# Performance work log

Hardware: AMD Instinct MI355X
Metric: run time of the kernel (lower is better)

The kernel has to match this reference:

```python
import jax, jax.numpy as jnp
import numpy as np

NUM_HEADS = 16

def setup_inputs() -> dict:
    key = jax.random.key(0)
    k1, k2, k3 = jax.random.split(key, 3)
    B, T, D = 4, 2048, 1024
    x = jax.random.normal(k1, (B, T, D), dtype=jnp.float32)
    # lecun_normal: std = 1/sqrt(fan_in)
    w = jax.random.normal(k2, (3 * D, D), dtype=jnp.float32) * (1.0 / np.sqrt(D))
    w_out = jax.random.normal(k3, (D, D), dtype=jnp.float32) * (1.0 / np.sqrt(D))
    return {"x": x, "w": w, "w_out": w_out}


def reference(x, w, w_out):
    B, T, D = x.shape
    H = NUM_HEADS
    L = D // H
    # qkv projection: (B,T,3D)
    q, k, v = jnp.split(jnp.matmul(x, w.T), 3, axis=2)
    # -> (T,B,H,L) time-major for the scan
    q = q.reshape(B, T, H, L).transpose(1, 0, 2, 3)
    k = k.reshape(B, T, H, L).transpose(1, 0, 2, 3)
    v = v.reshape(B, T, H, L).transpose(1, 0, 2, 3)
    scale = jax.lax.rsqrt(jnp.float32(L))
    k_exp = jnp.exp(k * scale) + 1e-6            # (T,B,H,L)
    k_norm = jnp.cumsum(k_exp, axis=0)           # causal normalizer
    qs = jax.nn.softmax(q * scale, axis=-1) / k_norm

    def step(carry, args):
        qs_t, k_t, v_t = args                    # each (B,H,L)
        # accumulate outer product k_t v_t^T into (B,H,L,L) state
        carry = carry + k_t[..., :, None] * v_t[..., None, :]
        y_t = jnp.einsum('bhl,bhlm->bhm', qs_t, carry)
        return carry, y_t

    init = jnp.zeros((B, H, L, L), dtype=x.dtype)
    _, y = jax.lax.scan(step, init, (qs, k_exp, v))   # y: (T,B,H,L)
    y = y.reshape(T, B, D).transpose(1, 0, 2)         # (B,T,D)
    return jnp.matmul(y, w_out)                       # Dense, no bias
```

## Files before the change

kernel.cpp:

```cpp
#include <hip/hip_runtime.h>
#include <math.h>

#define Bsz   4
#define Tsz   2048
#define Dsz   1024
#define Hsz   16
#define Lsz   64
#define BHsz  64
#define CH    64
#define NCH   32
#define QKVLD 3072
#define SCL   0.125f
#define QSC   512.0f
#define QSCI  (1.0f/512.0f)

typedef float  floatx4 __attribute__((ext_vector_type(4)));
typedef _Float16 half8 __attribute__((ext_vector_type(8)));
typedef _Float16 half4 __attribute__((ext_vector_type(4)));
typedef _Float16 half2v __attribute__((ext_vector_type(2)));

#define AS1 __attribute__((address_space(1)))
#define AS3 __attribute__((address_space(3)))

static __device__ __forceinline__ void gload_lds16(const void* g, void* l) {
  __builtin_amdgcn_global_load_lds((const AS1 unsigned int*)g,
                                   (AS3 unsigned int*)l, 16, 0, 0);
}

static __device__ __forceinline__ float wave_max64(float v) {
#pragma unroll
  for (int off = 1; off < 64; off <<= 1) v = fmaxf(v, __shfl_xor(v, off));
  return v;
}
static __device__ __forceinline__ float wave_sum64(float v) {
#pragma unroll
  for (int off = 1; off < 64; off <<= 1) v += __shfl_xor(v, off);
  return v;
}

__launch_bounds__(256)
__global__ void prep(const float* __restrict__ x, _Float16* __restrict__ xh,
                     const float* __restrict__ w, _Float16* __restrict__ wh,
                     const float* __restrict__ wo, _Float16* __restrict__ woT) {
  const int blk = blockIdx.x, tid = threadIdx.x;
  if (blk < 11264) {
    const float* in  = (blk < 8192) ? x : w;
    _Float16*   outp = (blk < 8192) ? xh : wh;
    const int bi = (blk < 8192) ? blk : blk - 8192;
    const int i = (bi * 256 + tid) * 4;
    float4 v = *(const float4*)(in + i);
    half4 h = { (_Float16)v.x, (_Float16)v.y, (_Float16)v.z, (_Float16)v.w };
    *(half4*)(outp + i) = h;
  } else {
    __shared__ float tile[32][33];
    const int bi = blk - 11264;
    const int bx = (bi & 31) * 32;
    const int by = (bi >> 5) * 32;
    const int tx = tid & 31, ty0 = tid >> 5;
#pragma unroll
    for (int p = 0; p < 4; p++) {
      const int ty = ty0 + p * 8;
      tile[ty][tx] = wo[(size_t)(by + ty) * 1024 + bx + tx];
    }
    __syncthreads();
#pragma unroll
    for (int p = 0; p < 4; p++) {
      const int ty = ty0 + p * 8;
      woT[(size_t)(bx + ty) * 1024 + by + tx] = (_Float16)tile[tx][ty];
    }
  }
}

__launch_bounds__(256)
__global__ void gemm_f16_bt_f32(const _Float16* __restrict__ A, const _Float16* __restrict__ B,
                                float* __restrict__ C, int M, int N, int K) {
  __shared__ _Float16 As[128][32];
  __shared__ _Float16 Bs[128][32];
  const int tid  = threadIdx.x;
  const int wave = tid >> 6, lane = tid & 63;
  const int flat = blockIdx.y * gridDim.x + blockIdx.x;
  const int xcd = flat & 7, g = flat >> 3;
  const int m0 = (xcd * 8 + (g & 7)) * 128;
  const int n0 = (g >> 3) * 128;
  const int wm = (wave >> 1) * 64, wn = (wave & 1) * 64;
  const int fr = lane & 15;
  const int fq = lane >> 4;
  const int lr = lane >> 2;
  const int lk = (lane & 3) * 8;

  floatx4 zero = {0.f, 0.f, 0.f, 0.f};
  floatx4 acc[4][4];
#pragma unroll
  for (int mt = 0; mt < 4; mt++)
#pragma unroll
    for (int nt = 0; nt < 4; nt++) acc[mt][nt] = zero;

  for (int k0 = 0; k0 < K; k0 += 32) {
    __syncthreads();
#pragma unroll
    for (int j = 0; j < 2; j++) {
      const int ia = wave * 2 + j;
      gload_lds16(A + (size_t)(m0 + ia * 16 + lr) * K + k0 + lk, &As[ia * 16][0]);
      gload_lds16(B + (size_t)(n0 + ia * 16 + lr) * K + k0 + lk, &Bs[ia * 16][0]);
    }
    __syncthreads();

    half8 af[4], bf[4];
#pragma unroll
    for (int i = 0; i < 4; i++) {
      af[i] = *(const half8*)&As[wm + i * 16 + fr][fq * 8];
      bf[i] = *(const half8*)&Bs[wn + i * 16 + fr][fq * 8];
    }
#pragma unroll
    for (int mt = 0; mt < 4; mt++)
#pragma unroll
      for (int nt = 0; nt < 4; nt++)
        acc[mt][nt] = __builtin_amdgcn_mfma_f32_16x16x32_f16(af[mt], bf[nt], acc[mt][nt], 0, 0, 0);
  }
#pragma unroll
  for (int mt = 0; mt < 4; mt++)
#pragma unroll
    for (int nt = 0; nt < 4; nt++)
#pragma unroll
      for (int r = 0; r < 4; r++) {
        const int row = m0 + wm + mt * 16 + fq * 4 + r;
        const int col = n0 + wn + nt * 16 + fr;
        C[(size_t)row * N + col] = acc[mt][nt][r];
      }
}

__launch_bounds__(256)
__global__ void gemm_f16_bt_c16(const _Float16* __restrict__ A, const _Float16* __restrict__ B,
                                _Float16* __restrict__ C, int M, int N, int K) {
  __shared__ _Float16 As[128][32];
  __shared__ _Float16 Bs[128][32];
  const int tid  = threadIdx.x;
  const int wave = tid >> 6, lane = tid & 63;
  const int flat = blockIdx.y * gridDim.x + blockIdx.x;
  const int xcd = flat & 7, g = flat >> 3;
  const int m0 = (xcd * 8 + (g & 7)) * 128;
  const int n0 = (g >> 3) * 128;
  const int wm = (wave >> 1) * 64, wn = (wave & 1) * 64;
  const int fr = lane & 15;
  const int fq = lane >> 4;
  const int lr = lane >> 2;
  const int lk = (lane & 3) * 8;
  const bool kreg = (n0 >= 1024) && (n0 < 2048);

  floatx4 zero = {0.f, 0.f, 0.f, 0.f};
  floatx4 acc[4][4];
#pragma unroll
  for (int mt = 0; mt < 4; mt++)
#pragma unroll
    for (int nt = 0; nt < 4; nt++) acc[mt][nt] = zero;

  for (int k0 = 0; k0 < K; k0 += 32) {
    __syncthreads();
#pragma unroll
    for (int j = 0; j < 2; j++) {
      const int ia = wave * 2 + j;
      gload_lds16(A + (size_t)(m0 + ia * 16 + lr) * K + k0 + lk, &As[ia * 16][0]);
      gload_lds16(B + (size_t)(n0 + ia * 16 + lr) * K + k0 + lk, &Bs[ia * 16][0]);
    }
    __syncthreads();

    half8 af[4], bf[4];
#pragma unroll
    for (int i = 0; i < 4; i++) {
      af[i] = *(const half8*)&As[wm + i * 16 + fr][fq * 8];
      bf[i] = *(const half8*)&Bs[wn + i * 16 + fr][fq * 8];
    }
#pragma unroll
    for (int mt = 0; mt < 4; mt++)
#pragma unroll
      for (int nt = 0; nt < 4; nt++)
        acc[mt][nt] = __builtin_amdgcn_mfma_f32_16x16x32_f16(af[mt], bf[nt], acc[mt][nt], 0, 0, 0);
  }
#pragma unroll
  for (int mt = 0; mt < 4; mt++)
#pragma unroll
    for (int nt = 0; nt < 4; nt++)
#pragma unroll
      for (int r = 0; r < 4; r++) {
        const int row = m0 + wm + mt * 16 + fq * 4 + r;
        const int col = n0 + wn + nt * 16 + fr;
        float v = acc[mt][nt][r];
        if (kreg) v = __expf(v * SCL) + 1e-6f;
        C[(size_t)row * N + col] = (_Float16)v;
      }
}

__launch_bounds__(256)
__global__ void chunk_kv(const _Float16* __restrict__ qkv, float* __restrict__ KV,
                         float* __restrict__ Ksum) {
  const int blk = blockIdx.x;
  const int bh = blk >> 3, cgrp = blk & 7;
  const int b = bh >> 4, h = bh & 15;
  const int tid = threadIdx.x;
  const int wave = tid >> 6, lane = tid & 63;
  const int fr = lane & 15, fq = lane >> 4;
  const int m2  = (tid & 31) * 2;
  const int tg8 = (tid >> 5) * 8;

  __shared__ __align__(16) _Float16 KxT[64][72];
  __shared__ __align__(16) _Float16 VT [64][72];

  for (int cc = 0; cc < 4; cc++) {
    const int c = cgrp * 4 + cc;
    const size_t base = ((size_t)(b * Tsz + c * CH)) * QKVLD + h * 64;
    __syncthreads();
    half8 klo, khi, vlo, vhi;
#pragma unroll
    for (int j = 0; j < 8; j++) {
      const int t = tg8 + j;
      half2v kk = *(const half2v*)(qkv + base + (size_t)t * QKVLD + 1024 + m2);
      klo[j] = kk[0]; khi[j] = kk[1];
      half2v vv = *(const half2v*)(qkv + base + (size_t)t * QKVLD + 2048 + m2);
      vlo[j] = vv[0]; vhi[j] = vv[1];
    }
    *(half8*)&KxT[m2][tg8]     = klo;
    *(half8*)&KxT[m2 + 1][tg8] = khi;
    *(half8*)&VT[m2][tg8]      = vlo;
    *(half8*)&VT[m2 + 1][tg8]  = vhi;
    __syncthreads();

    floatx4 acc[4];
#pragma unroll
    for (int j = 0; j < 4; j++) acc[j] = (floatx4){0.f, 0.f, 0.f, 0.f};
#pragma unroll
    for (int ks = 0; ks < 2; ks++) {
      half8 av = *(const half8*)&VT[wave * 16 + fr][ks * 32 + fq * 8];
#pragma unroll
      for (int j = 0; j < 4; j++) {
        half8 bv = *(const half8*)&KxT[j * 16 + fr][ks * 32 + fq * 8];
        acc[j] = __builtin_amdgcn_mfma_f32_16x16x32_f16(av, bv, acc[j], 0, 0, 0);
      }
    }
    float* KVp = KV + ((size_t)(bh * NCH + c)) * 4096;
#pragma unroll
    for (int j = 0; j < 4; j++)
#pragma unroll
      for (int r = 0; r < 4; r++)
        KVp[(wave * 16 + fq * 4 + r) * 64 + j * 16 + fr] = acc[j][r];

    if (tid < 64) {
      float s = 0.f;
      const half8* row = (const half8*)&KxT[tid][0];
#pragma unroll
      for (int j8 = 0; j8 < 8; j8++) {
        half8 v8 = row[j8];
#pragma unroll
        for (int j = 0; j < 8; j++) s += (float)v8[j];
      }
      Ksum[(bh * NCH + c) * 64 + tid] = s;
    }
  }
}

__launch_bounds__(256)
__global__ void prefix_kern(float* __restrict__ KV, float* __restrict__ Ksum) {
  const int tid = threadIdx.x;
  if (blockIdx.x < 256) {
    const int bh = blockIdx.x >> 2;
    const int e  = (blockIdx.x & 3) * 1024 + tid * 4;
    float4* p = (float4*)(KV + (size_t)bh * NCH * 4096 + e);
    float4 acc = {0.f, 0.f, 0.f, 0.f};
#pragma unroll 4
    for (int c = 0; c < NCH; c++) {
      float4 t = p[(size_t)c * 1024];
      p[(size_t)c * 1024] = acc;
      acc.x += t.x; acc.y += t.y; acc.z += t.z; acc.w += t.w;
    }
  } else {
    const int cid = (blockIdx.x - 256) * 256 + tid;
    const int bh = cid >> 4, l4 = cid & 15;
    float4* p = (float4*)(Ksum + (size_t)bh * NCH * 64) + l4;
    float4 acc = {0.f, 0.f, 0.f, 0.f};
#pragma unroll 4
    for (int c = 0; c < NCH; c++) {
      float4 t = p[c * 16];
      p[c * 16] = acc;
      acc.x += t.x; acc.y += t.y; acc.z += t.z; acc.w += t.w;
    }
  }
}

__launch_bounds__(256)
__global__ void chunk_y(const _Float16* __restrict__ qkv, const float* __restrict__ KV,
                        const float* __restrict__ Ksum, _Float16* __restrict__ Y) {
  const int bh = blockIdx.x, c = blockIdx.y;
  const int b = bh >> 4, h = bh & 15;
  const int tid = threadIdx.x;
  const int wave = tid >> 6, lane = tid & 63;
  const int fr = lane & 15, fq = lane >> 4;

  __shared__ __align__(16) _Float16 kxh[64][72];
  __shared__ __align__(16) _Float16 kxT[64][72];
  __shared__ __align__(16) _Float16 Ph[64][136];
  __shared__ __align__(16) _Float16 Bh[64][136];

  const size_t base = ((size_t)(b * Tsz + c * CH)) * QKVLD + h * 64;
  const float* KVp = KV + ((size_t)(bh * NCH + c)) * 4096;
  const int ksoff = (bh * NCH + c) * 64;

  _Float16 qreg[16];
#pragma unroll
  for (int i = 0; i < 16; i++)
    qreg[i] = qkv[base + (size_t)(wave * 16 + i) * QKVLD + lane];

  float ksb[4];
#pragma unroll
  for (int j = 0; j < 4; j++) ksb[j] = Ksum[ksoff + j * 16 + fr];

  {
    const int rr  = tid >> 3;
    const int sg8 = (tid & 7) * 8;
#pragma unroll
    for (int p = 0; p < 2; p++) {
      const int t = p * 32 + rr;
      *(half8*)&kxh[t][sg8] =
          *(const half8*)(qkv + base + (size_t)t * QKVLD + 1024 + sg8);
      *(half8*)&Ph[t][64 + sg8] =
          *(const half8*)(qkv + base + (size_t)t * QKVLD + 2048 + sg8);
    }
  }
  {
    const int m  = tid >> 2;
    const int l0 = (tid & 3) * 16;
#pragma unroll
    for (int q = 0; q < 2; q++) {
      float4 s0 = *(const float4*)(KVp + m * 64 + l0 + q * 8);
      float4 s1 = *(const float4*)(KVp + m * 64 + l0 + q * 8 + 4);
      half8 hh = { (_Float16)s0.x, (_Float16)s0.y, (_Float16)s0.z, (_Float16)s0.w,
                   (_Float16)s1.x, (_Float16)s1.y, (_Float16)s1.z, (_Float16)s1.w };
      *(half8*)&Bh[m][l0 + q * 8] = hh;
    }
  }
  __syncthreads();

  {
    const int l2  = (tid & 31) * 2;
    const int tg8 = (tid >> 5) * 8;
    half8 k0, k1, v0, v1;
#pragma unroll
    for (int j = 0; j < 8; j++) {
      const int t = tg8 + j;
      half2v kk = *(const half2v*)&kxh[t][l2];
      k0[j] = kk[0]; k1[j] = kk[1];
      half2v vv = *(const half2v*)&Ph[t][64 + l2];
      v0[j] = vv[0]; v1[j] = vv[1];
    }
    *(half8*)&kxT[l2][tg8]          = k0;
    *(half8*)&kxT[l2 + 1][tg8]      = k1;
    *(half8*)&Bh[l2][64 + tg8]      = v0;
    *(half8*)&Bh[l2 + 1][64 + tg8]  = v1;
  }
  __syncthreads();

  {
    floatx4 kacc[4];
#pragma unroll
    for (int j = 0; j < 4; j++) kacc[j] = (floatx4){0.f, 0.f, 0.f, 0.f};
#pragma unroll
    for (int ks = 0; ks < 2; ks++) {
      half8 af;
#pragma unroll
      for (int j = 0; j < 8; j++)
        af[j] = (ks * 32 + fq * 8 + j) <= (wave * 16 + fr) ? (_Float16)1.0f
                                                           : (_Float16)0.0f;
#pragma unroll
      for (int j = 0; j < 4; j++) {
        half8 bf = *(const half8*)&kxT[j * 16 + fr][ks * 32 + fq * 8];
        kacc[j] = __builtin_amdgcn_mfma_f32_16x16x32_f16(af, bf, kacc[j], 0, 0, 0);
      }
    }
    __syncthreads();
#pragma unroll
    for (int j = 0; j < 4; j++)
#pragma unroll
      for (int r = 0; r < 4; r++)
        kxT[wave * 16 + fq * 4 + r][j * 16 + fr] =
            (_Float16)(QSC / (ksb[j] + kacc[j][r]));
  }

#pragma unroll
  for (int i = 0; i < 16; i++) {
    const int t = wave * 16 + i;
    float v = (float)qreg[i] * SCL;
    float m = wave_max64(v);
    float e = __expf(v - m);
    float s = wave_sum64(e);
    Ph[t][lane] = (_Float16)((e / s) * (float)kxT[t][lane]);
  }
  __syncthreads();

  const int wm = (wave >> 1) * 32, wn = (wave & 1) * 32;
  {
    floatx4 a2[2][2];
#pragma unroll
    for (int mt = 0; mt < 2; mt++)
#pragma unroll
      for (int nt = 0; nt < 2; nt++) a2[mt][nt] = (floatx4){0.f, 0.f, 0.f, 0.f};
#pragma unroll
    for (int ks = 0; ks < 2; ks++) {
      half8 af[2], bf[2];
#pragma unroll
      for (int i = 0; i < 2; i++) {
        af[i] = *(const half8*)&Ph[wm + i * 16 + fr][ks * 32 + fq * 8];
        bf[i] = *(const half8*)&kxh[wn + i * 16 + fr][ks * 32 + fq * 8];
      }
#pragma unroll
      for (int mt = 0; mt < 2; mt++)
#pragma unroll
        for (int nt = 0; nt < 2; nt++)
          a2[mt][nt] = __builtin_amdgcn_mfma_f32_16x16x32_f16(af[mt], bf[nt], a2[mt][nt], 0, 0, 0);
    }
#pragma unroll
    for (int mt = 0; mt < 2; mt++)
#pragma unroll
      for (int nt = 0; nt < 2; nt++)
#pragma unroll
        for (int r = 0; r < 4; r++) {
          const int t = wm + mt * 16 + fq * 4 + r;
          const int s = wn + nt * 16 + fr;
          Ph[t][64 + s] = (_Float16)(s <= t ? a2[mt][nt][r] : 0.f);
        }
  }
  __syncthreads();

  {
    floatx4 acc[2][2];
#pragma unroll
    for (int mt = 0; mt < 2; mt++)
#pragma unroll
      for (int nt = 0; nt < 2; nt++) acc[mt][nt] = (floatx4){0.f, 0.f, 0.f, 0.f};
#pragma unroll
    for (int ks = 0; ks < 4; ks++) {
      half8 af[2], bf[2];
#pragma unroll
      for (int i = 0; i < 2; i++) {
        af[i] = *(const half8*)&Ph[wm + i * 16 + fr][ks * 32 + fq * 8];
        bf[i] = *(const half8*)&Bh[wn + i * 16 + fr][ks * 32 + fq * 8];
      }
#pragma unroll
      for (int mt = 0; mt < 2; mt++)
#pragma unroll
        for (int nt = 0; nt < 2; nt++)
          acc[mt][nt] = __builtin_amdgcn_mfma_f32_16x16x32_f16(af[mt], bf[nt], acc[mt][nt], 0, 0, 0);
    }
#pragma unroll
    for (int mt = 0; mt < 2; mt++)
#pragma unroll
      for (int nt = 0; nt < 2; nt++)
#pragma unroll
        for (int r = 0; r < 4; r++)
          kxh[wm + mt * 16 + fq * 4 + r][wn + nt * 16 + fr] =
              (_Float16)(acc[mt][nt][r] * QSCI);
  }
  __syncthreads();

  {
    const int ty = tid >> 2, sg = (tid & 3) * 16;
    _Float16* yrow = Y + (size_t)(b * Tsz + c * CH + ty) * Dsz + h * 64 + sg;
    *(half8*)(yrow)     = *(const half8*)&kxh[ty][sg];
    *(half8*)(yrow + 8) = *(const half8*)&kxh[ty][sg + 8];
  }
}

extern "C" void kernel_launch(void* const* d_in, const int* in_sizes, int n_in,
                              void* d_out, int out_size, void* d_ws, size_t ws_size,
                              hipStream_t stream) {
  const float* x     = (const float*)d_in[0];
  const float* w     = (const float*)d_in[1];
  const float* w_out = (const float*)d_in[2];
  float* out = (float*)d_out;

  _Float16* xh   = (_Float16*)d_ws;
  _Float16* Yh   = xh;
  _Float16* wh   = xh + (size_t)8192 * 1024;
  _Float16* woT  = wh + (size_t)3072 * 1024;
  _Float16* qkvh = woT + (size_t)1024 * 1024;
  float* KV   = (float*)(qkvh + (size_t)8192 * 3072);
  float* Ksum = KV + (size_t)BHsz * NCH * 4096;

  prep<<<12288, 256, 0, stream>>>(x, xh, w, wh, w_out, woT);

  gemm_f16_bt_c16<<<dim3(24, 64), 256, 0, stream>>>(xh, wh, qkvh, 8192, 3072, 1024);

  chunk_kv<<<512, 256, 0, stream>>>(qkvh, KV, Ksum);
  prefix_kern<<<260, 256, 0, stream>>>(KV, Ksum);
  chunk_y<<<dim3(BHsz, NCH), 256, 0, stream>>>(qkvh, KV, Ksum, Yh);

  gemm_f16_bt_f32<<<dim3(8, 64), 256, 0, stream>>>(Yh, woT, out, 8192, 1024, 1024);
}
```

Baseline: 257.7 us.

## Replace QKV projection GEMM with 256x256-tile double-buffered 8-wave pipelined kernel

Replaces the simple 128x128, K=32, single-buffered QKV GEMM with a 256x256-tile kernel that uses 512 threads, K=64 steps and two LDS buffers. Global-to-LDS loads for the next K slice are interleaved with the MFMA phases, and an XOR swizzle avoids LDS bank conflicts. The intent is to raise arithmetic intensity and hide memory latency in the largest GEMM. The cost is high register pressure from 32 accumulators per thread, large LDS use (128KB per block), and a hard-coded shape with a fragile hand-written wait/barrier schedule.

```diff
diff --git a/kernel.cpp b/kernel.cpp
--- a/kernel.cpp
+++ b/kernel.cpp
@@ -71,6 +71,127 @@
   }
 }
 
+__launch_bounds__(512, 2)
+__global__ void qkv_gemm8(const _Float16* __restrict__ A, const _Float16* __restrict__ B,
+                          _Float16* __restrict__ C) {
+  __shared__ __align__(16) _Float16 AsF[2 * 256 * 64];
+  __shared__ __align__(16) _Float16 BsF[2 * 256 * 64];
+  const int tid  = threadIdx.x;
+  const int wv   = tid >> 6, lane = tid & 63;
+  const int wm   = wv >> 2, wn = wv & 3;
+  const int fr   = lane & 15, fq = lane >> 4;
+
+  const int flat = blockIdx.x;
+  const int g  = (flat & 7) * 48 + (flat >> 3);
+  const int m0 = (g / 12) * 256;
+  const int n0 = (g % 12) * 256;
+
+  const int srow = lane >> 3;
+  const int scg  = (lane & 7) ^ srow;
+  const int wv8  = wv * 8;
+  const _Float16* aSrc = A + (size_t)(m0 + wv8 + srow) * 1024 + scg * 8;
+  const _Float16* bSrc = B + (size_t)(n0 + wv8 + srow) * 1024 + scg * 8;
+
+  const int sw  = fr & 7;
+  const int ck0 = ((0 + fq) ^ sw) * 8;
+  const int ck1 = ((4 + fq) ^ sw) * 8;
+  const _Float16* apt = AsF + (wm * 64 + fr) * 64;
+  const _Float16* bpt = BsF + (wn * 32 + fr) * 64;
+
+  floatx4 acc[8][4];
+#pragma unroll
+  for (int i = 0; i < 8; i++)
+#pragma unroll
+    for (int j = 0; j < 4; j++) acc[i][j] = (floatx4){0.f, 0.f, 0.f, 0.f};
+
+#define BAR() __builtin_amdgcn_s_barrier()
+#define VMW4() asm volatile("s_waitcnt vmcnt(4)" ::: "memory")
+
+#define STAGE_A(kt, hm, sbuf) do {                                             \
+    const _Float16* s_ = aSrc + (hm) * (128 * 1024) + (kt) * 64;               \
+    gload_lds16(s_,             &AsF[(sbuf) * 16384 + ((hm) * 128 + wv8) * 64]);      \
+    gload_lds16(s_ + 64 * 1024, &AsF[(sbuf) * 16384 + ((hm) * 128 + 64 + wv8) * 64]); \
+  } while (0)
+#define STAGE_B(kt, hm, sbuf) do {                                             \
+    const _Float16* s_ = bSrc + (hm) * (128 * 1024) + (kt) * 64;               \
+    gload_lds16(s_,             &BsF[(sbuf) * 16384 + ((hm) * 128 + wv8) * 64]);      \
+    gload_lds16(s_ + 64 * 1024, &BsF[(sbuf) * 16384 + ((hm) * 128 + 64 + wv8) * 64]); \
+  } while (0)
+
+#define PHASE(buf, qm, qn, STAGE_STMT) do {                                    \
+    half8 a0_[4], a1_[4], b0_[2], b1_[2];                                      \
+    _Pragma("unroll")                                                          \
+    for (int mf = 0; mf < 4; mf++) {                                           \
+      const _Float16* p_ = apt + (buf) * 16384 + (qm) * 8192 + mf * 1024;      \
+      a0_[mf] = *(const half8*)(p_ + ck0);                                     \
+      a1_[mf] = *(const half8*)(p_ + ck1);                                     \
+    }                                                                          \
+    _Pragma("unroll")                                                          \
+    for (int nf = 0; nf < 2; nf++) {                                           \
+      const _Float16* p_ = bpt + (buf) * 16384 + (qn) * 8192 + nf * 1024;      \
+      b0_[nf] = *(const half8*)(p_ + ck0);                                     \
+      b1_[nf] = *(const half8*)(p_ + ck1);                                     \
+    }                                                                          \
+    STAGE_STMT;                                                                \
+    __builtin_amdgcn_s_barrier();                                              \
+    asm volatile("s_waitcnt lgkmcnt(0)" ::: "memory");                         \
+    __builtin_amdgcn_sched_barrier(0);                                         \
+    __builtin_amdgcn_s_setprio(1);                                             \
+    _Pragma("unroll")                                                          \
+    for (int mf = 0; mf < 4; mf++)                                             \
+      _Pragma("unroll")                                                        \
+      for (int nf = 0; nf < 2; nf++) {                                         \
+        acc[(qm) * 4 + mf][(qn) * 2 + nf] = __builtin_amdgcn_mfma_f32_16x16x32_f16( \
+            a0_[mf], b0_[nf], acc[(qm) * 4 + mf][(qn) * 2 + nf], 0, 0, 0);     \
+        acc[(qm) * 4 + mf][(qn) * 2 + nf] = __builtin_amdgcn_mfma_f32_16x16x32_f16( \
+            a1_[mf], b1_[nf], acc[(qm) * 4 + mf][(qn) * 2 + nf], 0, 0, 0);     \
+      }                                                                        \
+    __builtin_amdgcn_s_setprio(0);                                             \
+  } while (0)
+
+  STAGE_A(0, 0, 0); STAGE_B(0, 1, 0); STAGE_A(0, 1, 0); STAGE_B(0, 0, 0);
+  STAGE_A(1, 0, 1); STAGE_B(1, 1, 1);
+  VMW4(); BAR();
+
+#pragma unroll 1
+  for (int t = 0; t < 16; t += 2) {
+    PHASE(0, 0, 0, STAGE_A(t + 1, 1, 1)); BAR();
+    PHASE(0, 0, 1, STAGE_B(t + 1, 0, 1)); BAR();
+    PHASE(0, 1, 1, STAGE_A(t + 2, 0, 0)); BAR();
+    PHASE(0, 1, 0, STAGE_B(t + 2, 1, 0)); VMW4(); BAR();
+    PHASE(1, 0, 0, STAGE_A(t + 2, 1, 0)); BAR();
+    PHASE(1, 0, 1, STAGE_B(t + 2, 0, 0)); BAR();
+    PHASE(1, 1, 1, STAGE_A(t + 3, 0, 1)); BAR();
+    PHASE(1, 1, 0, STAGE_B(t + 3, 1, 1)); VMW4(); BAR();
+  }
+
+#undef PHASE
+#undef STAGE_A
+#undef STAGE_B
+#undef VMW4
+#undef BAR
+
+  const bool kreg = (n0 >= 1024) && (n0 < 2048);
+#pragma unroll
+  for (int qm = 0; qm < 2; qm++)
+#pragma unroll
+    for (int mf = 0; mf < 4; mf++) {
+      const int row = m0 + qm * 128 + wm * 64 + mf * 16 + fq * 4;
+#pragma unroll
+      for (int qn = 0; qn < 2; qn++)
+#pragma unroll
+        for (int nf = 0; nf < 2; nf++) {
+          const int col = n0 + qn * 128 + wn * 32 + nf * 16 + fr;
+#pragma unroll
+          for (int r = 0; r < 4; r++) {
+            float v = acc[qm * 4 + mf][qn * 2 + nf][r];
+            if (kreg) v = __expf(v * SCL) + 1e-6f;
+            C[(size_t)(row + r) * 3072 + col] = (_Float16)v;
+          }
+        }
+    }
+}
+
 __launch_bounds__(256)
 __global__ void gemm_f16_bt_f32(const _Float16* __restrict__ A, const _Float16* __restrict__ B,
                                 float* __restrict__ C, int M, int N, int K) {
@@ -130,67 +251,6 @@
 }
 
 __launch_bounds__(256)
-__global__ void gemm_f16_bt_c16(const _Float16* __restrict__ A, const _Float16* __restrict__ B,
-                                _Float16* __restrict__ C, int M, int N, int K) {
-  __shared__ _Float16 As[128][32];
-  __shared__ _Float16 Bs[128][32];
-  const int tid  = threadIdx.x;
-  const int wave = tid >> 6, lane = tid & 63;
-  const int flat = blockIdx.y * gridDim.x + blockIdx.x;
-  const int xcd = flat & 7, g = flat >> 3;
-  const int m0 = (xcd * 8 + (g & 7)) * 128;
-  const int n0 = (g >> 3) * 128;
-  const int wm = (wave >> 1) * 64, wn = (wave & 1) * 64;
-  const int fr = lane & 15;
-  const int fq = lane >> 4;
-  const int lr = lane >> 2;
-  const int lk = (lane & 3) * 8;
-  const bool kreg = (n0 >= 1024) && (n0 < 2048);
-
-  floatx4 zero = {0.f, 0.f, 0.f, 0.f};
-  floatx4 acc[4][4];
-#pragma unroll
-  for (int mt = 0; mt < 4; mt++)
-#pragma unroll
-    for (int nt = 0; nt < 4; nt++) acc[mt][nt] = zero;
-
-  for (int k0 = 0; k0 < K; k0 += 32) {
-    __syncthreads();
-#pragma unroll
-    for (int j = 0; j < 2; j++) {
-      const int ia = wave * 2 + j;
-      gload_lds16(A + (size_t)(m0 + ia * 16 + lr) * K + k0 + lk, &As[ia * 16][0]);
-      gload_lds16(B + (size_t)(n0 + ia * 16 + lr) * K + k0 + lk, &Bs[ia * 16][0]);
-    }
-    __syncthreads();
-
-    half8 af[4], bf[4];
-#pragma unroll
-    for (int i = 0; i < 4; i++) {
-      af[i] = *(const half8*)&As[wm + i * 16 + fr][fq * 8];
-      bf[i] = *(const half8*)&Bs[wn + i * 16 + fr][fq * 8];
-    }
-#pragma unroll
-    for (int mt = 0; mt < 4; mt++)
-#pragma unroll
-      for (int nt = 0; nt < 4; nt++)
-        acc[mt][nt] = __builtin_amdgcn_mfma_f32_16x16x32_f16(af[mt], bf[nt], acc[mt][nt], 0, 0, 0);
-  }
-#pragma unroll
-  for (int mt = 0; mt < 4; mt++)
-#pragma unroll
-    for (int nt = 0; nt < 4; nt++)
-#pragma unroll
-      for (int r = 0; r < 4; r++) {
-        const int row = m0 + wm + mt * 16 + fq * 4 + r;
-        const int col = n0 + wn + nt * 16 + fr;
-        float v = acc[mt][nt][r];
-        if (kreg) v = __expf(v * SCL) + 1e-6f;
-        C[(size_t)row * N + col] = (_Float16)v;
-      }
-}
-
-__launch_bounds__(256)
 __global__ void chunk_kv(const _Float16* __restrict__ qkv, float* __restrict__ KV,
                          float* __restrict__ Ksum) {
   const int blk = blockIdx.x;
@@ -485,7 +545,7 @@
 
   prep<<<12288, 256, 0, stream>>>(x, xh, w, wh, w_out, woT);
 
-  gemm_f16_bt_c16<<<dim3(24, 64), 256, 0, stream>>>(xh, wh, qkvh, 8192, 3072, 1024);
+  qkv_gemm8<<<384, 512, 0, stream>>>(xh, wh, qkvh);
 
   chunk_kv<<<512, 256, 0, stream>>>(qkvh, KV, Ksum);
   prefix_kern<<<260, 256, 0, stream>>>(KV, Ksum);
```

After: 257.7 us. About the same (+0.0%).
